# Kernel optimization log

Hardware: AMD Instinct MI355X
Metric: run time of the kernel (lower is better)

The kernel has to match this reference:

```python
import jax, jax.numpy as jnp
import numpy as np

E, H, M, IN, T = 4, 64, 64, 32, 32      # e_size, hidden_state, message, in_size, target
HL = (128, 256, 128)                     # NNet hidden layers (priba's NNet default)
N_LAYERS = 3


def setup_inputs() -> dict:
    key = jax.random.key(0)
    ks = iter(jax.random.split(key, 64))
    B, N = 16, 128

    def w(shape, scale=0.1):
        return jax.random.normal(next(ks), shape, dtype=jnp.float32) * scale

    inp = {
        "h_in": jax.random.normal(next(ks), (B, N, IN), dtype=jnp.float32),
        "am": jax.random.normal(next(ks), (B, N, N, E), dtype=jnp.float32),
        "g_size": jax.random.randint(next(ks), (B,), 0, N),
    }
    # EdgeNetwork NNet: E -> 128 -> 256 -> 128 -> M*H
    dims_e = (E,) + HL + (M * H,)
    for i in range(4):
        inp[f"We{i}"] = w((dims_e[i], dims_e[i + 1]))
        inp[f"be{i}"] = w((dims_e[i + 1],))
    # GRU (torch nn.GRU, one layer, one step): input M, hidden H
    inp["Wih"] = w((3 * H, M)); inp["Whh"] = w((3 * H, H))
    inp["bih"] = w((3 * H,)); inp["bhh"] = w((3 * H,))
    # Readout NNets: i on [h_T, h_0] (H+IN -> T), j on h_T (H -> T)
    dims_i = (H + IN,) + HL + (T,)
    dims_j = (H,) + HL + (T,)
    for i in range(4):
        inp[f"Wi{i}"] = w((dims_i[i], dims_i[i + 1])); inp[f"bi{i}"] = w((dims_i[i + 1],))
        inp[f"Wj{i}"] = w((dims_j[i], dims_j[i + 1])); inp[f"bj{i}"] = w((dims_j[i + 1],))
    return inp


def _mlp(x, Ws, bs):
    for Wk, bk in zip(Ws[:-1], bs[:-1]):
        x = jax.nn.relu(x @ Wk + bk)
    return x @ Ws[-1] + bs[-1]


def reference(h_in, am, g_size,
              We0, be0, We1, be1, We2, be2, We3, be3,
              Wih, Whh, bih, bhh,
              Wi0, bi0, Wi1, bi1, Wi2, bi2, Wi3, bi3,
              Wj0, bj0, Wj1, bj1, Wj2, bj2, Wj3, bj3):
    B, N, _ = h_in.shape
    h = jnp.pad(h_in, ((0, 0), (0, 0), (0, H - IN)))            # pad to hidden size
    mask = (jnp.arange(N)[None, :] < g_size[:, None]).astype(h.dtype)[:, :, None]  # [B,N,1]

    # Edge-network hidden features; final linear layer is fused into the
    # message contraction to avoid materializing per-edge [M,H] matrices.
    f = am                                                       # [B,N,N,E]
    for Wk, bk in ((We0, be0), (We1, be1), (We2, be2)):
        f = jax.nn.relu(f @ Wk + bk)                             # [B,N,N,128]
    W3 = We3.reshape(HL[-1], M, H)                               # [128,M,H]
    b3 = be3.reshape(M, H)

    for _ in range(N_LAYERS):                                    # weight-tied GGNN steps
        # m[b,v,o] = sum_w (A(e_bvw) @ h_bw)[o], A = reshape(f @ We3 + be3)
        t = jnp.einsum('bvwk,bwi->bvki', f, h)                   # [B,N,128,H]
        msg = jnp.einsum('bvki,koi->bvo', t, W3)
        msg = msg + jnp.einsum('oi,bi->bo', b3, h.sum(1))[:, None, :]
        # single-step torch GRU update
        gi = msg @ Wih.T + bih
        gh = h @ Whh.T + bhh
        r = jax.nn.sigmoid(gi[..., :H] + gh[..., :H])
        z = jax.nn.sigmoid(gi[..., H:2 * H] + gh[..., H:2 * H])
        n = jnp.tanh(gi[..., 2 * H:] + r * gh[..., 2 * H:])
        h = (1.0 - z) * n + z * h
        h = h * mask

    # GGNN readout: sum_v mask * sigmoid(i([h_T, h_0])) * j(h_T), then log_softmax
    gate = jax.nn.sigmoid(_mlp(jnp.concatenate([h, h_in], -1),
                               (Wi0, Wi1, Wi2, Wi3), (bi0, bi1, bi2, bi3)))
    val = _mlp(h, (Wj0, Wj1, Wj2, Wj3), (bj0, bj1, bj2, bj3))
    res = (mask * gate * val).sum(1)                             # [B,T]
    return jax.nn.log_softmax(res, axis=1)
```

## Files before the change

kernel.cpp:

```cpp
#include <hip/hip_runtime.h>
#include <math.h>

#define B   16
#define N   128
#define E   4
#define H   64
#define M   64
#define IN_ 32
#define T   32
#define K1  128
#define K2  256
#define K3  128

typedef _Float16 f16;
typedef f16  f16x8 __attribute__((ext_vector_type(8)));
typedef float f32x4 __attribute__((ext_vector_type(4)));

#define MFMA16(a, b, c) __builtin_amdgcn_mfma_f32_16x16x32_f16(a, b, c, 0, 0, 0)

__global__ __launch_bounds__(256) void pad_h_kernel(const float* __restrict__ h_in,
                                                    float* __restrict__ h,
                                                    f16* __restrict__ h16) {
    int idx = blockIdx.x * 256 + threadIdx.x;
    if (idx >= B * N * H) return;
    int i  = idx & (H - 1);
    int bn = idx >> 6;
    float v = (i < IN_) ? h_in[bn * IN_ + i] : 0.f;
    h[idx] = v;
    h16[idx] = (f16)v;
}

__global__ __launch_bounds__(256) void prep_weights(
    const float* __restrict__ We1, const float* __restrict__ We2,
    const float* __restrict__ We3,
    f16* __restrict__ W1t, f16* __restrict__ W2t, f16* __restrict__ We3h) {
    int idx = blockIdx.x * 256 + threadIdx.x;
    if (idx < 32768) {
        int j = idx >> 7, k = idx & 127;
        W1t[idx] = (f16)We1[k * 256 + j];
    } else if (idx < 65536) {
        int t = idx - 32768;
        int j = t >> 8, k = t & 255;
        W2t[t] = (f16)We2[k * 128 + j];
    } else {
        int t = idx - 65536;
        if (t < 524288) We3h[t] = (f16)We3[t];
    }
}

__global__ __launch_bounds__(256, 2) void edge_mlp_mfma(
    const float* __restrict__ am,
    const float* __restrict__ We0, const float* __restrict__ be0,
    const f16* __restrict__ W1t, const float* __restrict__ be1,
    const f16* __restrict__ W2t, const float* __restrict__ be2,
    f16* __restrict__ f) {
    __shared__ float xl[64][4];
    __shared__ f16 y1[64][136];
    __shared__ f16 y2[64][264];
    int tid = threadIdx.x;
    int lane = tid & 63, wv = tid >> 6;
    long long g0 = (long long)blockIdx.x * 64;

    ((float*)xl)[tid] = am[g0 * 4 + tid];
    __syncthreads();

    {
        int j = tid & 127, e0 = (tid >> 7) * 32;
        float w0 = We0[j], w1 = We0[128 + j], w2 = We0[256 + j], w3 = We0[384 + j];
        float bb = be0[j];
        #pragma unroll 8
        for (int e = e0; e < e0 + 32; ++e) {
            float v = bb + xl[e][0] * w0 + xl[e][1] * w1
                         + xl[e][2] * w2 + xl[e][3] * w3;
            y1[e][j] = (f16)fmaxf(v, 0.f);
        }
    }
    __syncthreads();

    int m = lane & 15, q = lane >> 4;

    {
        f32x4 acc[4][4];
        #pragma unroll
        for (int ct = 0; ct < 4; ++ct)
            #pragma unroll
            for (int rt = 0; rt < 4; ++rt) acc[ct][rt] = (f32x4){0.f, 0.f, 0.f, 0.f};
        #pragma unroll
        for (int s = 0; s < 4; ++s) {
            int k0 = s * 32 + q * 8;
            f16x8 afr[4], bfr[4];
            #pragma unroll
            for (int rt = 0; rt < 4; ++rt)
                afr[rt] = *(const f16x8*)&y1[rt * 16 + m][k0];
            #pragma unroll
            for (int ct = 0; ct < 4; ++ct) {
                int n = (wv * 4 + ct) * 16 + m;
                bfr[ct] = *(const f16x8*)(W1t + n * 128 + k0);
            }
            #pragma unroll
            for (int ct = 0; ct < 4; ++ct)
                #pragma unroll
                for (int rt = 0; rt < 4; ++rt)
                    acc[ct][rt] = MFMA16(afr[rt], bfr[ct], acc[ct][rt]);
        }
        #pragma unroll
        for (int ct = 0; ct < 4; ++ct) {
            int n = (wv * 4 + ct) * 16 + m;
            float bb = be1[n];
            #pragma unroll
            for (int rt = 0; rt < 4; ++rt)
                #pragma unroll
                for (int r = 0; r < 4; ++r) {
                    int row = rt * 16 + q * 4 + r;
                    y2[row][n] = (f16)fmaxf(acc[ct][rt][r] + bb, 0.f);
                }
        }
    }
    __syncthreads();

    {
        f32x4 acc[2][4];
        #pragma unroll
        for (int ct = 0; ct < 2; ++ct)
            #pragma unroll
            for (int rt = 0; rt < 4; ++rt) acc[ct][rt] = (f32x4){0.f, 0.f, 0.f, 0.f};
        #pragma unroll
        for (int s = 0; s < 8; ++s) {
            int k0 = s * 32 + q * 8;
            f16x8 afr[4], bfr[2];
            #pragma unroll
            for (int rt = 0; rt < 4; ++rt)
                afr[rt] = *(const f16x8*)&y2[rt * 16 + m][k0];
            #pragma unroll
            for (int ct = 0; ct < 2; ++ct) {
                int n = (wv * 2 + ct) * 16 + m;
                bfr[ct] = *(const f16x8*)(W2t + n * 256 + k0);
            }
            #pragma unroll
            for (int ct = 0; ct < 2; ++ct)
                #pragma unroll
                for (int rt = 0; rt < 4; ++rt)
                    acc[ct][rt] = MFMA16(afr[rt], bfr[ct], acc[ct][rt]);
        }
        #pragma unroll
        for (int ct = 0; ct < 2; ++ct) {
            int n = (wv * 2 + ct) * 16 + m;
            float bb = be2[n];
            #pragma unroll
            for (int rt = 0; rt < 4; ++rt)
                #pragma unroll
                for (int r = 0; r < 4; ++r) {
                    int row = rt * 16 + q * 4 + r;
                    y1[row][n] = (f16)fmaxf(acc[ct][rt][r] + bb, 0.f);
                }
        }
    }
    __syncthreads();

    #pragma unroll
    for (int j = 0; j < 4; ++j) {
        int c = tid + j * 256;
        int e = c >> 4, p = c & 15;
        *(uint4*)(f + (g0 + e) * 128 + p * 8) = *(const uint4*)&y1[e][p * 8];
    }
}

__global__ __launch_bounds__(256) void msg_init_kernel(
    const float* __restrict__ h, const float* __restrict__ be3,
    float* __restrict__ msgb) {
    __shared__ float part[4][64];
    __shared__ float hsum[64];
    __shared__ float bias[64];
    int tid = threadIdx.x;
    int b = blockIdx.x;
    int i = tid & 63, wq = tid >> 6;
    float s = 0.f;
    for (int w = wq; w < N; w += 4) s += h[((size_t)(b * N + w)) * H + i];
    part[wq][i] = s;
    __syncthreads();
    if (tid < 64) hsum[tid] = part[0][tid] + part[1][tid] + part[2][tid] + part[3][tid];
    __syncthreads();
    if (tid < 64) {
        float sb = 0.f;
        #pragma unroll 4
        for (int ii = 0; ii < H; ++ii) sb += be3[tid * H + ii] * hsum[ii];
        bias[tid] = sb;
    }
    __syncthreads();
    for (int idx = tid; idx < N * M; idx += 256)
        msgb[(size_t)b * N * M + idx] = bias[idx & 63];
}

__global__ __launch_bounds__(256, 2) void p_gemm(
    const f16* __restrict__ h16, const f16* __restrict__ We3h,
    f16* __restrict__ P2) {
    __shared__ f16 Al[128][72];
    __shared__ f16 Bl[128][72];
    __shared__ f16 Ol[128][136];
    int tid = threadIdx.x, lane = tid & 63, wv = tid >> 6;
    int ob = blockIdx.x;
    int nt = blockIdx.y;

    #pragma unroll
    for (int j = 0; j < 4; ++j) {
        int c = tid + j * 256;
        int row = c >> 3, p = c & 7;
        *(uint4*)&Al[row][p * 8] =
            *(const uint4*)(h16 + (size_t)(nt * 128 + row) * 64 + p * 8);
    }
    #pragma unroll
    for (int j = 0; j < 4; ++j) {
        int c = tid + j * 256;
        int k = c >> 3, p = c & 7;
        *(uint4*)&Bl[k][p * 8] =
            *(const uint4*)(We3h + ((size_t)(k * 64 + ob)) * 64 + p * 8);
    }
    __syncthreads();

    int m = lane & 15, q = lane >> 4;
    f32x4 acc[2][8];
    #pragma unroll
    for (int ct = 0; ct < 2; ++ct)
        #pragma unroll
        for (int rt = 0; rt < 8; ++rt) acc[ct][rt] = (f32x4){0.f, 0.f, 0.f, 0.f};
    #pragma unroll
    for (int s = 0; s < 2; ++s) {
        int k0 = s * 32 + q * 8;
        f16x8 afr[8], bfr[2];
        #pragma unroll
        for (int rt = 0; rt < 8; ++rt)
            afr[rt] = *(const f16x8*)&Al[rt * 16 + m][k0];
        #pragma unroll
        for (int ct = 0; ct < 2; ++ct)
            bfr[ct] = *(const f16x8*)&Bl[(wv * 2 + ct) * 16 + m][k0];
        #pragma unroll
        for (int ct = 0; ct < 2; ++ct)
            #pragma unroll
            for (int rt = 0; rt < 8; ++rt)
                acc[ct][rt] = MFMA16(afr[rt], bfr[ct], acc[ct][rt]);
    }
    #pragma unroll
    for (int ct = 0; ct < 2; ++ct) {
        int col = (wv * 2 + ct) * 16 + m;
        #pragma unroll
        for (int rt = 0; rt < 8; ++rt)
            #pragma unroll
            for (int r = 0; r < 4; ++r)
                Ol[rt * 16 + q * 4 + r][col] = (f16)acc[ct][rt][r];
    }
    __syncthreads();
    #pragma unroll
    for (int j = 0; j < 8; ++j) {
        int c = tid + j * 256;
        int row = c >> 4, p = c & 15;
        *(uint4*)(P2 + ((size_t)(nt * 128 + row) * 64 + ob) * 128 + p * 8) =
            *(const uint4*)&Ol[row][p * 8];
    }
}

__global__ __launch_bounds__(256, 2) void msg_mfma(
    const f16* __restrict__ f, const f16* __restrict__ P2,
    float* __restrict__ part) {
    __shared__ f16 Al[128][136];
    __shared__ f16 Bl[64][136];
    int tid = threadIdx.x, lane = tid & 63, wv = tid >> 6;
    int ws = blockIdx.x;
    int b  = blockIdx.y;
    int m = lane & 15, q = lane >> 4;

    f32x4 acc[2][4];
    #pragma unroll
    for (int rt = 0; rt < 2; ++rt)
        #pragma unroll
        for (int ct = 0; ct < 4; ++ct) acc[rt][ct] = (f32x4){0.f, 0.f, 0.f, 0.f};

    for (int wi = 0; wi < 4; ++wi) {
        int w = ws * 4 + wi;
        #pragma unroll
        for (int j = 0; j < 8; ++j) {
            int c = tid + j * 256;
            int v = c >> 4, p = c & 15;
            *(uint4*)&Al[v][p * 8] =
                *(const uint4*)(f + (((size_t)(b * 128 + v) * 128 + w) * 128) + p * 8);
        }
        #pragma unroll
        for (int j = 0; j < 4; ++j) {
            int c = tid + j * 256;
            int o = c >> 4, p = c & 15;
            *(uint4*)&Bl[o][p * 8] =
                *(const uint4*)(P2 + (((size_t)(b * 128 + w) * 64 + o) * 128) + p * 8);
        }
        __syncthreads();
        #pragma unroll
        for (int s = 0; s < 4; ++s) {
            int k0 = s * 32 + q * 8;
            f16x8 afr[2], bfr[4];
            #pragma unroll
            for (int rt = 0; rt < 2; ++rt)
                afr[rt] = *(const f16x8*)&Al[(wv * 2 + rt) * 16 + m][k0];
            #pragma unroll
            for (int ct = 0; ct < 4; ++ct)
                bfr[ct] = *(const f16x8*)&Bl[ct * 16 + m][k0];
            #pragma unroll
            for (int rt = 0; rt < 2; ++rt)
                #pragma unroll
                for (int ct = 0; ct < 4; ++ct)
                    acc[rt][ct] = MFMA16(afr[rt], bfr[ct], acc[rt][ct]);
        }
        __syncthreads();
    }
    float* pp = part + (size_t)ws * (2048 * 64);
    #pragma unroll
    for (int rt = 0; rt < 2; ++rt)
        #pragma unroll
        for (int ct = 0; ct < 4; ++ct) {
            int o = ct * 16 + m;
            #pragma unroll
            for (int r = 0; r < 4; ++r) {
                int v = (wv * 2 + rt) * 16 + q * 4 + r;
                pp[(size_t)(b * 128 + v) * 64 + o] = acc[rt][ct][r];
            }
        }
}

__global__ __launch_bounds__(192) void gru_kernel(
    const float* __restrict__ msgb, const float* __restrict__ part,
    float* __restrict__ h, f16* __restrict__ h16,
    const float* __restrict__ Wih, const float* __restrict__ Whh,
    const float* __restrict__ bih, const float* __restrict__ bhh,
    const int* __restrict__ g_size) {
    __shared__ float m_lds[M];
    __shared__ float h_lds[H];
    __shared__ float gi[3 * H], gh[3 * H];
    int tid = threadIdx.x;
    int bv  = blockIdx.x;
    int b = bv >> 7, v = bv & 127;

    if (tid < M) {
        float s = msgb[bv * M + tid];
        #pragma unroll 8
        for (int sp = 0; sp < 32; ++sp)
            s += part[(size_t)sp * (2048 * 64) + bv * 64 + tid];
        m_lds[tid] = s;
    } else if (tid < M + H) {
        h_lds[tid - M] = h[bv * H + (tid - M)];
    }
    __syncthreads();

    {
        float si = bih[tid], sh = bhh[tid];
        const float* wi = Wih + tid * M;
        const float* wh = Whh + tid * H;
        #pragma unroll 4
        for (int k = 0; k < M; ++k) si += wi[k] * m_lds[k];
        #pragma unroll 4
        for (int k = 0; k < H; ++k) sh += wh[k] * h_lds[k];
        gi[tid] = si;
        gh[tid] = sh;
    }
    __syncthreads();
    if (tid < H) {
        float r = 1.f / (1.f + expf(-(gi[tid] + gh[tid])));
        float z = 1.f / (1.f + expf(-(gi[H + tid] + gh[H + tid])));
        float n = tanhf(gi[2 * H + tid] + r * gh[2 * H + tid]);
        float hv = (1.f - z) * n + z * h_lds[tid];
        float maskf = (v < g_size[b]) ? 1.f : 0.f;
        hv *= maskf;
        h[bv * H + tid] = hv;
        h16[bv * H + tid] = (f16)hv;
    }
}

__global__ __launch_bounds__(256) void readout_kernel(
    const float* __restrict__ h, const float* __restrict__ h_in,
    const int* __restrict__ g_size,
    const float* __restrict__ Wi0, const float* __restrict__ bi0,
    const float* __restrict__ Wi1, const float* __restrict__ bi1,
    const float* __restrict__ Wi2, const float* __restrict__ bi2,
    const float* __restrict__ Wi3, const float* __restrict__ bi3,
    const float* __restrict__ Wj0, const float* __restrict__ bj0,
    const float* __restrict__ Wj1, const float* __restrict__ bj1,
    const float* __restrict__ Wj2, const float* __restrict__ bj2,
    const float* __restrict__ Wj3, const float* __restrict__ bj3,
    float* __restrict__ contrib) {
    __shared__ float x[H + IN_];
    __shared__ float a1[128], a2[256], a3[128];
    __shared__ float gate[T];
    int tid = threadIdx.x;
    int bv  = blockIdx.x;
    int b = bv >> 7, v = bv & 127;

    if (tid < H) x[tid] = h[bv * H + tid];
    else if (tid < H + IN_) x[tid] = h_in[bv * IN_ + (tid - H)];
    __syncthreads();

    if (tid < 128) {
        float s = bi0[tid];
        #pragma unroll 4
        for (int c = 0; c < 96; ++c) s += x[c] * Wi0[c * 128 + tid];
        a1[tid] = fmaxf(s, 0.f);
    }
    __syncthreads();
    {
        float s = bi1[tid];
        #pragma unroll 4
        for (int k = 0; k < 128; ++k) s += a1[k] * Wi1[k * 256 + tid];
        a2[tid] = fmaxf(s, 0.f);
    }
    __syncthreads();
    if (tid < 128) {
        float s = bi2[tid];
        #pragma unroll 4
        for (int k = 0; k < 256; ++k) s += a2[k] * Wi2[k * 128 + tid];
        a3[tid] = fmaxf(s, 0.f);
    }
    __syncthreads();
    if (tid < T) {
        float s = bi3[tid];
        #pragma unroll 4
        for (int k = 0; k < 128; ++k) s += a3[k] * Wi3[k * T + tid];
        gate[tid] = 1.f / (1.f + expf(-s));
    }
    __syncthreads();

    if (tid < 128) {
        float s = bj0[tid];
        #pragma unroll 4
        for (int c = 0; c < 64; ++c) s += x[c] * Wj0[c * 128 + tid];
        a1[tid] = fmaxf(s, 0.f);
    }
    __syncthreads();
    {
        float s = bj1[tid];
        #pragma unroll 4
        for (int k = 0; k < 128; ++k) s += a1[k] * Wj1[k * 256 + tid];
        a2[tid] = fmaxf(s, 0.f);
    }
    __syncthreads();
    if (tid < 128) {
        float s = bj2[tid];
        #pragma unroll 4
        for (int k = 0; k < 256; ++k) s += a2[k] * Wj2[k * 128 + tid];
        a3[tid] = fmaxf(s, 0.f);
    }
    __syncthreads();
    if (tid < T) {
        float s = bj3[tid];
        #pragma unroll 4
        for (int k = 0; k < 128; ++k) s += a3[k] * Wj3[k * T + tid];
        float maskf = (v < g_size[b]) ? 1.f : 0.f;
        contrib[bv * T + tid] = maskf * gate[tid] * s;
    }
}

__global__ __launch_bounds__(64) void finalize_kernel(const float* __restrict__ contrib,
                                                      float* __restrict__ out) {
    __shared__ float res[T];
    int b = blockIdx.x;
    int o = threadIdx.x;
    if (o < T) {
        float s = 0.f;
        for (int v = 0; v < N; ++v) s += contrib[(b * N + v) * T + o];
        res[o] = s;
    }
    __syncthreads();
    if (o < T) {
        float mx = res[0];
        for (int i = 1; i < T; ++i) mx = fmaxf(mx, res[i]);
        float se = 0.f;
        for (int i = 0; i < T; ++i) se += expf(res[i] - mx);
        out[b * T + o] = res[o] - mx - logf(se);
    }
}

extern "C" void kernel_launch(void* const* d_in, const int* in_sizes, int n_in,
                              void* d_out, int out_size, void* d_ws, size_t ws_size,
                              hipStream_t stream) {
    (void)in_sizes; (void)n_in; (void)out_size; (void)ws_size;
    const float* h_in = (const float*)d_in[0];
    const float* am   = (const float*)d_in[1];
    const int*   g_sz = (const int*)d_in[2];
    const float* We0 = (const float*)d_in[3],  *be0 = (const float*)d_in[4];
    const float* We1 = (const float*)d_in[5],  *be1 = (const float*)d_in[6];
    const float* We2 = (const float*)d_in[7],  *be2 = (const float*)d_in[8];
    const float* We3 = (const float*)d_in[9],  *be3 = (const float*)d_in[10];
    const float* Wih = (const float*)d_in[11], *Whh = (const float*)d_in[12];
    const float* bih = (const float*)d_in[13], *bhh = (const float*)d_in[14];
    const float* Wi0 = (const float*)d_in[15], *bi0 = (const float*)d_in[16];
    const float* Wj0 = (const float*)d_in[17], *bj0 = (const float*)d_in[18];
    const float* Wi1 = (const float*)d_in[19], *bi1 = (const float*)d_in[20];
    const float* Wj1 = (const float*)d_in[21], *bj1 = (const float*)d_in[22];
    const float* Wi2 = (const float*)d_in[23], *bi2 = (const float*)d_in[24];
    const float* Wj2 = (const float*)d_in[25], *bj2 = (const float*)d_in[26];
    const float* Wi3 = (const float*)d_in[27], *bi3 = (const float*)d_in[28];
    const float* Wj3 = (const float*)d_in[29], *bj3 = (const float*)d_in[30];

    float* out = (float*)d_out;

    f16*   f    = (f16*)d_ws;
    f16*   P2   = f + (size_t)33554432;
    float* part = (float*)(P2 + (size_t)16777216);
    float* h    = part + (size_t)4194304;
    float* msgb = h + 131072;
    float* contrib = msgb + 131072;
    f16*   h16  = (f16*)(contrib + 65536);
    f16*   W1t  = h16 + 131072;
    f16*   W2t  = W1t + 32768;
    f16*   We3h = W2t + 32768;

    pad_h_kernel<<<(B * N * H) / 256, 256, 0, stream>>>(h_in, h, h16);
    prep_weights<<<(65536 + 524288) / 256, 256, 0, stream>>>(We1, We2, We3,
                                                             W1t, W2t, We3h);
    edge_mlp_mfma<<<(B * N * N) / 64, 256, 0, stream>>>(am, We0, be0, W1t, be1,
                                                        W2t, be2, f);
    for (int l = 0; l < 3; ++l) {
        msg_init_kernel<<<B, 256, 0, stream>>>(h, be3, msgb);
        p_gemm<<<dim3(64, 16), 256, 0, stream>>>(h16, We3h, P2);
        msg_mfma<<<dim3(32, 16), 256, 0, stream>>>(f, P2, part);
        gru_kernel<<<B * N, 192, 0, stream>>>(msgb, part, h, h16,
                                              Wih, Whh, bih, bhh, g_sz);
    }
    readout_kernel<<<B * N, 256, 0, stream>>>(h, h_in, g_sz,
                                              Wi0, bi0, Wi1, bi1, Wi2, bi2, Wi3, bi3,
                                              Wj0, bj0, Wj1, bj1, Wj2, bj2, Wj3, bj3,
                                              contrib);
    finalize_kernel<<<B, 64, 0, stream>>>(contrib, out);
}
```

Before: 474.0 us.

## Rewrite readout MLPs as batched fp16 MFMA kernel over 32-node tiles

Replaces the per-node scalar fp32 readout kernel (one block per node, rereading every weight matrix from global memory) with a kernel that processes 32 nodes per block using 16x16x32 fp16 MFMA. Readout weights are pre-transposed and cast to fp16 in the existing weight-prep pass, and h_in is also stored as fp16. This cuts redundant weight traffic and scalar FMA work in the readout stage. In exchange it adds a larger prep kernel and lowers readout precision to fp16, and the readout grid shrinks to only 64 blocks.

```diff
diff --git a/kernel.cpp b/kernel.cpp
--- a/kernel.cpp
+++ b/kernel.cpp
@@ -18,9 +18,23 @@
 
 #define MFMA16(a, b, c) __builtin_amdgcn_mfma_f32_16x16x32_f16(a, b, c, 0, 0, 0)
 
+#define OFF_W1T   0
+#define OFF_W2T   32768
+#define OFF_WE3H  65536
+#define OFF_RI0   589824
+#define OFF_RI1   602112
+#define OFF_RI2   634880
+#define OFF_RI3   667648
+#define OFF_RJ0   671744
+#define OFF_RJ1   679936
+#define OFF_RJ2   712704
+#define OFF_RJ3   745472
+#define WPACK_SZ  749568
+
 __global__ __launch_bounds__(256) void pad_h_kernel(const float* __restrict__ h_in,
                                                     float* __restrict__ h,
-                                                    f16* __restrict__ h16) {
+                                                    f16* __restrict__ h16,
+                                                    f16* __restrict__ hin16) {
     int idx = blockIdx.x * 256 + threadIdx.x;
     if (idx >= B * N * H) return;
     int i  = idx & (H - 1);
@@ -28,23 +42,61 @@
     float v = (i < IN_) ? h_in[bn * IN_ + i] : 0.f;
     h[idx] = v;
     h16[idx] = (f16)v;
+    if (i < IN_) hin16[bn * IN_ + i] = (f16)v;
 }
 
 __global__ __launch_bounds__(256) void prep_weights(
     const float* __restrict__ We1, const float* __restrict__ We2,
     const float* __restrict__ We3,
-    f16* __restrict__ W1t, f16* __restrict__ W2t, f16* __restrict__ We3h) {
+    const float* __restrict__ Wi0, const float* __restrict__ Wi1,
+    const float* __restrict__ Wi2, const float* __restrict__ Wi3,
+    const float* __restrict__ Wj0, const float* __restrict__ Wj1,
+    const float* __restrict__ Wj2, const float* __restrict__ Wj3,
+    f16* __restrict__ wp) {
     int idx = blockIdx.x * 256 + threadIdx.x;
-    if (idx < 32768) {
-        int j = idx >> 7, k = idx & 127;
-        W1t[idx] = (f16)We1[k * 256 + j];
-    } else if (idx < 65536) {
-        int t = idx - 32768;
+    if (idx < OFF_W2T) {
+        int t = idx;
+        int j = t >> 7, k = t & 127;
+        wp[idx] = (f16)We1[k * 256 + j];
+    } else if (idx < OFF_WE3H) {
+        int t = idx - OFF_W2T;
         int j = t >> 8, k = t & 255;
-        W2t[t] = (f16)We2[k * 128 + j];
-    } else {
-        int t = idx - 65536;
-        if (t < 524288) We3h[t] = (f16)We3[t];
+        wp[idx] = (f16)We2[k * 128 + j];
+    } else if (idx < OFF_RI0) {
+        int t = idx - OFF_WE3H;
+        wp[idx] = (f16)We3[t];
+    } else if (idx < OFF_RI1) {
+        int t = idx - OFF_RI0;
+        int n = t / 96, c = t % 96;
+        wp[idx] = (f16)Wi0[c * 128 + n];
+    } else if (idx < OFF_RI2) {
+        int t = idx - OFF_RI1;
+        int n = t >> 7, k = t & 127;
+        wp[idx] = (f16)Wi1[k * 256 + n];
+    } else if (idx < OFF_RI3) {
+        int t = idx - OFF_RI2;
+        int n = t >> 8, k = t & 255;
+        wp[idx] = (f16)Wi2[k * 128 + n];
+    } else if (idx < OFF_RJ0) {
+        int t = idx - OFF_RI3;
+        int n = t >> 7, k = t & 127;
+        wp[idx] = (f16)Wi3[k * 32 + n];
+    } else if (idx < OFF_RJ1) {
+        int t = idx - OFF_RJ0;
+        int n = t >> 6, c = t & 63;
+        wp[idx] = (f16)Wj0[c * 128 + n];
+    } else if (idx < OFF_RJ2) {
+        int t = idx - OFF_RJ1;
+        int n = t >> 7, k = t & 127;
+        wp[idx] = (f16)Wj1[k * 256 + n];
+    } else if (idx < OFF_RJ3) {
+        int t = idx - OFF_RJ2;
+        int n = t >> 8, k = t & 255;
+        wp[idx] = (f16)Wj2[k * 128 + n];
+    } else if (idx < WPACK_SZ) {
+        int t = idx - OFF_RJ3;
+        int n = t >> 7, k = t & 127;
+        wp[idx] = (f16)Wj3[k * 32 + n];
     }
 }
 
@@ -371,85 +423,294 @@
     }
 }
 
-__global__ __launch_bounds__(256) void readout_kernel(
-    const float* __restrict__ h, const float* __restrict__ h_in,
+__global__ __launch_bounds__(256, 4) void readout_mfma(
+    const f16* __restrict__ h16, const f16* __restrict__ hin16,
     const int* __restrict__ g_size,
-    const float* __restrict__ Wi0, const float* __restrict__ bi0,
-    const float* __restrict__ Wi1, const float* __restrict__ bi1,
-    const float* __restrict__ Wi2, const float* __restrict__ bi2,
-    const float* __restrict__ Wi3, const float* __restrict__ bi3,
-    const float* __restrict__ Wj0, const float* __restrict__ bj0,
-    const float* __restrict__ Wj1, const float* __restrict__ bj1,
-    const float* __restrict__ Wj2, const float* __restrict__ bj2,
-    const float* __restrict__ Wj3, const float* __restrict__ bj3,
+    const f16* __restrict__ Ri0, const float* __restrict__ bi0,
+    const f16* __restrict__ Ri1, const float* __restrict__ bi1,
+    const f16* __restrict__ Ri2, const float* __restrict__ bi2,
+    const f16* __restrict__ Ri3, const float* __restrict__ bi3,
+    const f16* __restrict__ Rj0, const float* __restrict__ bj0,
+    const f16* __restrict__ Rj1, const float* __restrict__ bj1,
+    const f16* __restrict__ Rj2, const float* __restrict__ bj2,
+    const f16* __restrict__ Rj3, const float* __restrict__ bj3,
     float* __restrict__ contrib) {
-    __shared__ float x[H + IN_];
-    __shared__ float a1[128], a2[256], a3[128];
-    __shared__ float gate[T];
-    int tid = threadIdx.x;
-    int bv  = blockIdx.x;
-    int b = bv >> 7, v = bv & 127;
-
-    if (tid < H) x[tid] = h[bv * H + tid];
-    else if (tid < H + IN_) x[tid] = h_in[bv * IN_ + (tid - H)];
-    __syncthreads();
-
-    if (tid < 128) {
-        float s = bi0[tid];
-        #pragma unroll 4
-        for (int c = 0; c < 96; ++c) s += x[c] * Wi0[c * 128 + tid];
-        a1[tid] = fmaxf(s, 0.f);
-    }
-    __syncthreads();
-    {
-        float s = bi1[tid];
-        #pragma unroll 4
-        for (int k = 0; k < 128; ++k) s += a1[k] * Wi1[k * 256 + tid];
-        a2[tid] = fmaxf(s, 0.f);
-    }
-    __syncthreads();
-    if (tid < 128) {
-        float s = bi2[tid];
-        #pragma unroll 4
-        for (int k = 0; k < 256; ++k) s += a2[k] * Wi2[k * 128 + tid];
-        a3[tid] = fmaxf(s, 0.f);
-    }
-    __syncthreads();
-    if (tid < T) {
-        float s = bi3[tid];
-        #pragma unroll 4
-        for (int k = 0; k < 128; ++k) s += a3[k] * Wi3[k * T + tid];
-        gate[tid] = 1.f / (1.f + expf(-s));
-    }
-    __syncthreads();
-
-    if (tid < 128) {
-        float s = bj0[tid];
-        #pragma unroll 4
-        for (int c = 0; c < 64; ++c) s += x[c] * Wj0[c * 128 + tid];
-        a1[tid] = fmaxf(s, 0.f);
-    }
-    __syncthreads();
-    {
-        float s = bj1[tid];
-        #pragma unroll 4
-        for (int k = 0; k < 128; ++k) s += a1[k] * Wj1[k * 256 + tid];
-        a2[tid] = fmaxf(s, 0.f);
-    }
-    __syncthreads();
-    if (tid < 128) {
-        float s = bj2[tid];
-        #pragma unroll 4
-        for (int k = 0; k < 256; ++k) s += a2[k] * Wj2[k * 128 + tid];
-        a3[tid] = fmaxf(s, 0.f);
-    }
-    __syncthreads();
-    if (tid < T) {
-        float s = bj3[tid];
-        #pragma unroll 4
-        for (int k = 0; k < 128; ++k) s += a3[k] * Wj3[k * T + tid];
-        float maskf = (v < g_size[b]) ? 1.f : 0.f;
-        contrib[bv * T + tid] = maskf * gate[tid] * s;
+    __shared__ f16 Xl[32][104];
+    __shared__ f16 A1[32][136];
+    __shared__ f16 A2[32][264];
+    __shared__ float Gl[32][36];
+    int tid = threadIdx.x, lane = tid & 63, wv = tid >> 6;
+    int m = lane & 15, q = lane >> 4;
+    int r0 = blockIdx.x * 32;
+
+    {
+        int row = tid >> 3, p = tid & 7;
+        *(uint4*)&Xl[row][p * 8] = *(const uint4*)(h16 + (size_t)(r0 + row) * 64 + p * 8);
+        if (tid < 128) {
+            int row2 = tid >> 2, p2 = tid & 3;
+            *(uint4*)&Xl[row2][64 + p2 * 8] =
+                *(const uint4*)(hin16 + (size_t)(r0 + row2) * 32 + p2 * 8);
+        }
+    }
+    __syncthreads();
+
+    {
+        f32x4 acc[2][2];
+        #pragma unroll
+        for (int ct = 0; ct < 2; ++ct)
+            #pragma unroll
+            for (int rt = 0; rt < 2; ++rt) acc[ct][rt] = (f32x4){0.f, 0.f, 0.f, 0.f};
+        #pragma unroll
+        for (int s = 0; s < 3; ++s) {
+            int k0 = s * 32 + q * 8;
+            f16x8 afr[2], bfr[2];
+            #pragma unroll
+            for (int rt = 0; rt < 2; ++rt) afr[rt] = *(const f16x8*)&Xl[rt * 16 + m][k0];
+            #pragma unroll
+            for (int ct = 0; ct < 2; ++ct)
+                bfr[ct] = *(const f16x8*)(Ri0 + ((wv * 2 + ct) * 16 + m) * 96 + k0);
+            #pragma unroll
+            for (int ct = 0; ct < 2; ++ct)
+                #pragma unroll
+                for (int rt = 0; rt < 2; ++rt)
+                    acc[ct][rt] = MFMA16(afr[rt], bfr[ct], acc[ct][rt]);
+        }
+        #pragma unroll
+        for (int ct = 0; ct < 2; ++ct) {
+            int n = (wv * 2 + ct) * 16 + m;
+            float bb = bi0[n];
+            #pragma unroll
+            for (int rt = 0; rt < 2; ++rt)
+                #pragma unroll
+                for (int r = 0; r < 4; ++r)
+                    A1[rt * 16 + q * 4 + r][n] = (f16)fmaxf(acc[ct][rt][r] + bb, 0.f);
+        }
+    }
+    __syncthreads();
+
+    {
+        f32x4 acc[4][2];
+        #pragma unroll
+        for (int ct = 0; ct < 4; ++ct)
+            #pragma unroll
+            for (int rt = 0; rt < 2; ++rt) acc[ct][rt] = (f32x4){0.f, 0.f, 0.f, 0.f};
+        #pragma unroll
+        for (int s = 0; s < 4; ++s) {
+            int k0 = s * 32 + q * 8;
+            f16x8 afr[2], bfr[4];
+            #pragma unroll
+            for (int rt = 0; rt < 2; ++rt) afr[rt] = *(const f16x8*)&A1[rt * 16 + m][k0];
+            #pragma unroll
+            for (int ct = 0; ct < 4; ++ct)
+                bfr[ct] = *(const f16x8*)(Ri1 + ((wv * 4 + ct) * 16 + m) * 128 + k0);
+            #pragma unroll
+            for (int ct = 0; ct < 4; ++ct)
+                #pragma unroll
+                for (int rt = 0; rt < 2; ++rt)
+                    acc[ct][rt] = MFMA16(afr[rt], bfr[ct], acc[ct][rt]);
+        }
+        #pragma unroll
+        for (int ct = 0; ct < 4; ++ct) {
+            int n = (wv * 4 + ct) * 16 + m;
+            float bb = bi1[n];
+            #pragma unroll
+            for (int rt = 0; rt < 2; ++rt)
+                #pragma unroll
+                for (int r = 0; r < 4; ++r)
+                    A2[rt * 16 + q * 4 + r][n] = (f16)fmaxf(acc[ct][rt][r] + bb, 0.f);
+        }
+    }
+    __syncthreads();
+
+    {
+        f32x4 acc[2][2];
+        #pragma unroll
+        for (int ct = 0; ct < 2; ++ct)
+            #pragma unroll
+            for (int rt = 0; rt < 2; ++rt) acc[ct][rt] = (f32x4){0.f, 0.f, 0.f, 0.f};
+        #pragma unroll
+        for (int s = 0; s < 8; ++s) {
+            int k0 = s * 32 + q * 8;
+            f16x8 afr[2], bfr[2];
+            #pragma unroll
+            for (int rt = 0; rt < 2; ++rt) afr[rt] = *(const f16x8*)&A2[rt * 16 + m][k0];
+            #pragma unroll
+            for (int ct = 0; ct < 2; ++ct)
+                bfr[ct] = *(const f16x8*)(Ri2 + ((wv * 2 + ct) * 16 + m) * 256 + k0);
+            #pragma unroll
+            for (int ct = 0; ct < 2; ++ct)
+                #pragma unroll
+                for (int rt = 0; rt < 2; ++rt)
+                    acc[ct][rt] = MFMA16(afr[rt], bfr[ct], acc[ct][rt]);
+        }
+        __syncthreads();
+        #pragma unroll
+        for (int ct = 0; ct < 2; ++ct) {
+            int n = (wv * 2 + ct) * 16 + m;
+            float bb = bi2[n];
+            #pragma unroll
+            for (int rt = 0; rt < 2; ++rt)
+                #pragma unroll
+                for (int r = 0; r < 4; ++r)
+                    A1[rt * 16 + q * 4 + r][n] = (f16)fmaxf(acc[ct][rt][r] + bb, 0.f);
+        }
+    }
+    __syncthreads();
+
+    if (wv < 2) {
+        f32x4 acc[2];
+        acc[0] = (f32x4){0.f, 0.f, 0.f, 0.f};
+        acc[1] = (f32x4){0.f, 0.f, 0.f, 0.f};
+        int n = wv * 16 + m;
+        #pragma unroll
+        for (int s = 0; s < 4; ++s) {
+            int k0 = s * 32 + q * 8;
+            f16x8 bfr = *(const f16x8*)(Ri3 + n * 128 + k0);
+            #pragma unroll
+            for (int rt = 0; rt < 2; ++rt) {
+                f16x8 afr = *(const f16x8*)&A1[rt * 16 + m][k0];
+                acc[rt] = MFMA16(afr, bfr, acc[rt]);
+            }
+        }
+        float bb = bi3[n];
+        #pragma unroll
+        for (int rt = 0; rt < 2; ++rt)
+            #pragma unroll
+            for (int r = 0; r < 4; ++r)
+                Gl[rt * 16 + q * 4 + r][n] = 1.f / (1.f + expf(-(acc[rt][r] + bb)));
+    }
+    __syncthreads();
+
+    {
+        f32x4 acc[2][2];
+        #pragma unroll
+        for (int ct = 0; ct < 2; ++ct)
+            #pragma unroll
+            for (int rt = 0; rt < 2; ++rt) acc[ct][rt] = (f32x4){0.f, 0.f, 0.f, 0.f};
+        #pragma unroll
+        for (int s = 0; s < 2; ++s) {
+            int k0 = s * 32 + q * 8;
+            f16x8 afr[2], bfr[2];
+            #pragma unroll
+            for (int rt = 0; rt < 2; ++rt) afr[rt] = *(const f16x8*)&Xl[rt * 16 + m][k0];
+            #pragma unroll
+            for (int ct = 0; ct < 2; ++ct)
+                bfr[ct] = *(const f16x8*)(Rj0 + ((wv * 2 + ct) * 16 + m) * 64 + k0);
+            #pragma unroll
+            for (int ct = 0; ct < 2; ++ct)
+                #pragma unroll
+                for (int rt = 0; rt < 2; ++rt)
+                    acc[ct][rt] = MFMA16(afr[rt], bfr[ct], acc[ct][rt]);
+        }
+        __syncthreads();
+        #pragma unroll
+        for (int ct = 0; ct < 2; ++ct) {
+            int n = (wv * 2 + ct) * 16 + m;
+            float bb = bj0[n];
+            #pragma unroll
+            for (int rt = 0; rt < 2; ++rt)
+                #pragma unroll
+                for (int r = 0; r < 4; ++r)
+                    A1[rt * 16 + q * 4 + r][n] = (f16)fmaxf(acc[ct][rt][r] + bb, 0.f);
+        }
+    }
+    __syncthreads();
+
+    {
+        f32x4 acc[4][2];
+        #pragma unroll
+        for (int ct = 0; ct < 4; ++ct)
+            #pragma unroll
+            for (int rt = 0; rt < 2; ++rt) acc[ct][rt] = (f32x4){0.f, 0.f, 0.f, 0.f};
+        #pragma unroll
+        for (int s = 0; s < 4; ++s) {
+            int k0 = s * 32 + q * 8;
+            f16x8 afr[2], bfr[4];
+            #pragma unroll
+            for (int rt = 0; rt < 2; ++rt) afr[rt] = *(const f16x8*)&A1[rt * 16 + m][k0];
+            #pragma unroll
+            for (int ct = 0; ct < 4; ++ct)
+                bfr[ct] = *(const f16x8*)(Rj1 + ((wv * 4 + ct) * 16 + m) * 128 + k0);
+            #pragma unroll
+            for (int ct = 0; ct < 4; ++ct)
+                #pragma unroll
+                for (int rt = 0; rt < 2; ++rt)
+                    acc[ct][rt] = MFMA16(afr[rt], bfr[ct], acc[ct][rt]);
+        }
+        #pragma unroll
+        for (int ct = 0; ct < 4; ++ct) {
+            int n = (wv * 4 + ct) * 16 + m;
+            float bb = bj1[n];
+            #pragma unroll
+            for (int rt = 0; rt < 2; ++rt)
+                #pragma unroll
+                for (int r = 0; r < 4; ++r)
+                    A2[rt * 16 + q * 4 + r][n] = (f16)fmaxf(acc[ct][rt][r] + bb, 0.f);
+        }
+    }
+    __syncthreads();
+
+    {
+        f32x4 acc[2][2];
+        #pragma unroll
+        for (int ct = 0; ct < 2; ++ct)
+            #pragma unroll
+            for (int rt = 0; rt < 2; ++rt) acc[ct][rt] = (f32x4){0.f, 0.f, 0.f, 0.f};
+        #pragma unroll
+        for (int s = 0; s < 8; ++s) {
+            int k0 = s * 32 + q * 8;
+            f16x8 afr[2], bfr[2];
+            #pragma unroll
+            for (int rt = 0; rt < 2; ++rt) afr[rt] = *(const f16x8*)&A2[rt * 16 + m][k0];
+            #pragma unroll
+            for (int ct = 0; ct < 2; ++ct)
+                bfr[ct] = *(const f16x8*)(Rj2 + ((wv * 2 + ct) * 16 + m) * 256 + k0);
+            #pragma unroll
+            for (int ct = 0; ct < 2; ++ct)
+                #pragma unroll
+                for (int rt = 0; rt < 2; ++rt)
+                    acc[ct][rt] = MFMA16(afr[rt], bfr[ct], acc[ct][rt]);
+        }
+        __syncthreads();
+        #pragma unroll
+        for (int ct = 0; ct < 2; ++ct) {
+            int n = (wv * 2 + ct) * 16 + m;
+            float bb = bj2[n];
+            #pragma unroll
+            for (int rt = 0; rt < 2; ++rt)
+                #pragma unroll
+                for (int r = 0; r < 4; ++r)
+                    A1[rt * 16 + q * 4 + r][n] = (f16)fmaxf(acc[ct][rt][r] + bb, 0.f);
+        }
+    }
+    __syncthreads();
+
+    if (wv < 2) {
+        f32x4 acc[2];
+        acc[0] = (f32x4){0.f, 0.f, 0.f, 0.f};
+        acc[1] = (f32x4){0.f, 0.f, 0.f, 0.f};
+        int n = wv * 16 + m;
+        #pragma unroll
+        for (int s = 0; s < 4; ++s) {
+            int k0 = s * 32 + q * 8;
+            f16x8 bfr = *(const f16x8*)(Rj3 + n * 128 + k0);
+            #pragma unroll
+            for (int rt = 0; rt < 2; ++rt) {
+                f16x8 afr = *(const f16x8*)&A1[rt * 16 + m][k0];
+                acc[rt] = MFMA16(afr, bfr, acc[rt]);
+            }
+        }
+        float bb = bj3[n];
+        #pragma unroll
+        for (int rt = 0; rt < 2; ++rt)
+            #pragma unroll
+            for (int r = 0; r < 4; ++r) {
+                int row = rt * 16 + q * 4 + r;
+                int rg = r0 + row;
+                int b = rg >> 7, v = rg & 127;
+                float maskf = (v < g_size[b]) ? 1.f : 0.f;
+                contrib[(size_t)rg * T + n] = maskf * Gl[row][n] * (acc[rt][r] + bb);
+            }
     }
 }
 
@@ -504,13 +765,25 @@
     float* msgb = h + 131072;
     float* contrib = msgb + 131072;
     f16*   h16  = (f16*)(contrib + 65536);
-    f16*   W1t  = h16 + 131072;
-    f16*   W2t  = W1t + 32768;
-    f16*   We3h = W2t + 32768;
-
-    pad_h_kernel<<<(B * N * H) / 256, 256, 0, stream>>>(h_in, h, h16);
-    prep_weights<<<(65536 + 524288) / 256, 256, 0, stream>>>(We1, We2, We3,
-                                                             W1t, W2t, We3h);
+    f16*   hin16 = h16 + 131072;
+    f16*   wp   = hin16 + 65536;
+
+    f16* W1t  = wp + OFF_W1T;
+    f16* W2t  = wp + OFF_W2T;
+    f16* We3h = wp + OFF_WE3H;
+    f16* Ri0  = wp + OFF_RI0;
+    f16* Ri1  = wp + OFF_RI1;
+    f16* Ri2  = wp + OFF_RI2;
+    f16* Ri3  = wp + OFF_RI3;
+    f16* Rj0  = wp + OFF_RJ0;
+    f16* Rj1  = wp + OFF_RJ1;
+    f16* Rj2  = wp + OFF_RJ2;
+    f16* Rj3  = wp + OFF_RJ3;
+
+    pad_h_kernel<<<(B * N * H) / 256, 256, 0, stream>>>(h_in, h, h16, hin16);
+    prep_weights<<<WPACK_SZ / 256, 256, 0, stream>>>(We1, We2, We3,
+                                                     Wi0, Wi1, Wi2, Wi3,
+                                                     Wj0, Wj1, Wj2, Wj3, wp);
     edge_mlp_mfma<<<(B * N * N) / 64, 256, 0, stream>>>(am, We0, be0, W1t, be1,
                                                         W2t, be2, f);
     for (int l = 0; l < 3; ++l) {
@@ -520,9 +793,9 @@
         gru_kernel<<<B * N, 192, 0, stream>>>(msgb, part, h, h16,
                                               Wih, Whh, bih, bhh, g_sz);
     }
-    readout_kernel<<<B * N, 256, 0, stream>>>(h, h_in, g_sz,
-                                              Wi0, bi0, Wi1, bi1, Wi2, bi2, Wi3, bi3,
-                                              Wj0, bj0, Wj1, bj1, Wj2, bj2, Wj3, bj3,
-                                              contrib);
+    readout_mfma<<<64, 256, 0, stream>>>(h16, hin16, g_sz,
+                                         Ri0, bi0, Ri1, bi1, Ri2, bi2, Ri3, bi3,
+                                         Rj0, bj0, Rj1, bj1, Rj2, bj2, Rj3, bj3,
+                                         contrib);
     finalize_kernel<<<B, 64, 0, stream>>>(contrib, out);
 }
```

New measurement: 414.7 us. 1.14x faster.
